# Performance work log

Measured on AMD Instinct MI355X. Metric: run time of the kernel, lower is better.

Reference implementation:

```python
import jax, jax.numpy as jnp
import numpy as np

B, S, D, H = 2, 2048, 1024, 16
HD = D // H


def setup_inputs() -> dict:
    key = jax.random.key(0)
    ks = jax.random.split(key, 5)
    scale = 0.02
    x = jax.random.normal(ks[0], (B, S, D), dtype=jnp.float32)
    Wq = jax.random.normal(ks[1], (D, D), dtype=jnp.float32) * scale
    Wk = jax.random.normal(ks[2], (D, D), dtype=jnp.float32) * scale
    Wv = jax.random.normal(ks[3], (D, D), dtype=jnp.float32) * scale
    Wo = jax.random.normal(ks[4], (D, D), dtype=jnp.float32) * scale
    z = jnp.zeros((D,), dtype=jnp.float32)
    return {"x": x, "Wq": Wq, "bq": z, "Wk": Wk, "bk": z, "Wv": Wv, "bv": z, "Wo": Wo, "bo": z}


def reference(x, Wq, bq, Wk, bk, Wv, bv, Wo, bo):
    b, s, d = x.shape
    hd = d // H
    # QKV projections -> [b, H, s, hd]
    def heads(W, bias):
        return (x @ W.T + bias).reshape(b, s, H, hd).transpose(0, 2, 1, 3)
    q = heads(Wq, bq)
    k = heads(Wk, bk)
    v = heads(Wv, bv)
    scale = 1.0 / np.sqrt(hd).astype(np.float32)
    attn = scale * jnp.einsum('bhqd,bhkd->bhqk', q, k)  # [b,H,s,s]
    # causal mask (attn dropout p=0 is identity before masking)
    causal = jnp.tril(jnp.ones((s, s), dtype=bool))
    attn = jnp.where(causal[None, None], attn, -jnp.inf)
    attn = jax.nn.softmax(attn, axis=-1)
    ans = jnp.einsum('bhqk,bhkd->bhqd', attn, v)
    ans = ans.transpose(0, 2, 1, 3).reshape(b, s, d)
    return ans @ Wo.T + bo
```

## Files before the change

### kernel.cpp

```cpp
#include <hip/hip_runtime.h>

#define DEV __device__ __forceinline__

typedef __attribute__((ext_vector_type(8))) __bf16 bf16x8;
typedef __attribute__((ext_vector_type(4))) float f32x4;
typedef __attribute__((ext_vector_type(16))) float f32x16;
typedef __attribute__((ext_vector_type(4))) unsigned short u16x4;
typedef __attribute__((ext_vector_type(8))) unsigned short u16x8;
typedef __attribute__((ext_vector_type(2))) unsigned u32x2;

DEV unsigned short f2bf(float f) {
  unsigned u = __builtin_bit_cast(unsigned, f);
  u += 0x7FFFu + ((u >> 16) & 1u);
  return (unsigned short)(u >> 16);
}

DEV f32x4 mfma16(bf16x8 a, bf16x8 b, f32x4 c) {
  return __builtin_amdgcn_mfma_f32_16x16x32_bf16(a, b, c, 0, 0, 0);
}
DEV f32x16 mfma32(bf16x8 a, bf16x8 b, f32x16 c) {
  return __builtin_amdgcn_mfma_f32_32x32x16_bf16(a, b, c, 0, 0, 0);
}

DEV void gload16(const void* g, void* l) {
  __builtin_amdgcn_global_load_lds(
      (const __attribute__((address_space(1))) unsigned int*)g,
      (__attribute__((address_space(3))) unsigned int*)l, 16, 0, 0);
}

DEV void plswap(unsigned& x, unsigned& y) {
#if __has_builtin(__builtin_amdgcn_permlane32_swap)
  u32x2 r = __builtin_amdgcn_permlane32_swap(x, y, false, false);
  x = r[0];
  y = r[1];
#else
  unsigned sx = __shfl_xor(x, 32, 64), sy = __shfl_xor(y, 32, 64);
  int hi = (threadIdx.x & 63) >> 5;
  unsigned nx = hi ? sy : x;
  unsigned ny = hi ? y : sx;
  x = nx;
  y = ny;
#endif
}
DEV float xadd32(float v) {
  unsigned a = __builtin_bit_cast(unsigned, v), b = a;
  plswap(a, b);
  return __builtin_bit_cast(float, a) + __builtin_bit_cast(float, b);
}

__global__ __launch_bounds__(256) void k_cvt_all(
    const float* __restrict__ x,
    const float* __restrict__ Wq, const float* __restrict__ Wk,
    const float* __restrict__ Wv, const float* __restrict__ Wo,
    unsigned short* __restrict__ xb,
    unsigned short* __restrict__ Wqb, unsigned short* __restrict__ Wkb,
    unsigned short* __restrict__ Wvb, unsigned short* __restrict__ Wob) {
  int g = blockIdx.x * 256 + threadIdx.x;
  const float* src;
  unsigned short* dst;
  int loc;
  if (g < 524288) {
    src = x; dst = xb; loc = g;
  } else {
    int r = g - 524288;
    int w = r >> 17;
    loc = r & 131071;
    src = w == 0 ? Wq : w == 1 ? Wk : w == 2 ? Wv : Wo;
    dst = w == 0 ? Wqb : w == 1 ? Wkb : w == 2 ? Wvb : Wob;
  }
  int row = loc >> 7, k8 = loc & 127;
  const f32x4* s = (const f32x4*)(src + ((size_t)row << 10) + (k8 << 3));
  f32x4 a = s[0], b = s[1];
  u16x8 o;
  o[0] = f2bf(a[0]); o[1] = f2bf(a[1]); o[2] = f2bf(a[2]); o[3] = f2bf(a[3]);
  o[4] = f2bf(b[0]); o[5] = f2bf(b[1]); o[6] = f2bf(b[2]); o[7] = f2bf(b[3]);
  *(u16x8*)(dst + ((size_t)row << 10) + ((k8 << 3) ^ ((row & 7) << 3))) = o;
}

DEV void gemm_mainloop(const char* Ag, const char* Bg, char* lds,
                       int lane, int wid, f32x4 acc[4][4]) {
  int g4 = lane >> 4, r16 = lane & 15;
  int wm = wid >> 1, wn = wid & 1;
  int adA[2], adB[2];
#pragma unroll
  for (int ks = 0; ks < 2; ++ks) {
    int swz = ((ks * 4 + g4) ^ (lane & 7)) << 4;
    adA[ks] = (wm * 64 + r16) * 128 + swz;
    adB[ks] = 16384 + (wn * 64 + r16) * 128 + swz;
  }
  int o0 = wid * 4096 + lane * 16;
  int grow[4], ginr[4];
#pragma unroll
  for (int i = 0; i < 4; ++i) {
    grow[i] = (o0 + i * 1024) >> 7;
    ginr[i] = (o0 + i * 1024) & 127;
  }
  auto STAGE = [&](int KT, int BASE) {
#pragma unroll
    for (int i = 0; i < 4; ++i) {
      int oo = o0 + i * 1024;
      size_t gofs = (size_t)grow[i] * 2048 + (size_t)KT * 128 + ginr[i];
      gload16(Ag + gofs, lds + BASE + oo);
      gload16(Bg + gofs, lds + BASE + 16384 + oo);
    }
  };
  STAGE(0, 0);
  __syncthreads();
  for (int kt = 0; kt < 16; ++kt) {
    int cur = (kt & 1) << 15;
    if (kt + 1 < 16) STAGE(kt + 1, cur ^ 32768);
#pragma unroll
    for (int ks = 0; ks < 2; ++ks) {
      bf16x8 af[4], bfr[4];
#pragma unroll
      for (int i = 0; i < 4; ++i) {
        af[i]  = *(const bf16x8*)(lds + cur + adA[ks] + i * 2048);
        bfr[i] = *(const bf16x8*)(lds + cur + adB[ks] + i * 2048);
      }
#pragma unroll
      for (int mi = 0; mi < 4; ++mi)
#pragma unroll
        for (int ni = 0; ni < 4; ++ni)
          acc[mi][ni] = mfma16(af[mi], bfr[ni], acc[mi][ni]);
    }
    __syncthreads();
  }
}

__global__ __launch_bounds__(256) void k_gemm_qkv(
    const unsigned short* __restrict__ xb,
    const unsigned short* __restrict__ Wqb, const unsigned short* __restrict__ Wkb,
    const unsigned short* __restrict__ Wvb,
    const float* __restrict__ bq, const float* __restrict__ bk,
    const float* __restrict__ bv,
    unsigned short* __restrict__ Qb, unsigned short* __restrict__ Kb,
    unsigned short* __restrict__ Vt) {
  __shared__ char lds[65536];
  int tid = threadIdx.x, lane = tid & 63, wid = tid >> 6;
  int bm = blockIdx.x & 31, bn = blockIdx.x >> 5;
  int r0 = bm * 128;
  int colT = bn * 128;
  int which = colT >> 10;
  int ncol = colT & 1023;
  const unsigned short* Wb = which == 0 ? Wqb : which == 1 ? Wkb : Wvb;
  f32x4 acc[4][4] = {};
  gemm_mainloop((const char*)xb + (size_t)r0 * 2048,
                (const char*)Wb + (size_t)ncol * 2048, lds, lane, wid, acc);
  int g4 = lane >> 4, r16 = lane & 15, wm = wid >> 1, wn = wid & 1;
  const float* bias = which == 0 ? bq : which == 1 ? bk : bv;
  float oscale = which == 0 ? 0.18033688f : 1.0f;
  int ncolw = ncol + wn * 64;
#pragma unroll
  for (int ni = 0; ni < 4; ++ni) {
    int gcol = ncolw + ni * 16 + r16;
    float bvv = bias[gcol];
    int h = gcol >> 6, hd = gcol & 63;
#pragma unroll
    for (int mi = 0; mi < 4; ++mi) {
      int growb = r0 + wm * 64 + mi * 16 + g4 * 4;
      int bb = growb >> 11, s0 = growb & 2047;
      if (which == 2) {
        u16x4 pk;
#pragma unroll
        for (int jj = 0; jj < 4; ++jj) pk[jj] = f2bf(acc[mi][ni][jj] + bvv);
        *(u16x4*)(Vt + ((size_t)(bb * 16 + h) * 64 + hd) * 2048 + s0) = pk;
      } else {
        unsigned short* dst = which == 0 ? Qb : Kb;
        size_t base = ((size_t)(bb * 16 + h) * 2048 + s0) * 64 + hd;
#pragma unroll
        for (int jj = 0; jj < 4; ++jj)
          dst[base + (size_t)jj * 64] = f2bf((acc[mi][ni][jj] + bvv) * oscale);
      }
    }
  }
}

__global__ __launch_bounds__(128) void k_attn(
    const unsigned short* __restrict__ Q, const unsigned short* __restrict__ K,
    const unsigned short* __restrict__ Vt, unsigned short* __restrict__ ansb,
    float* __restrict__ PO, float* __restrict__ PL) {
  __shared__ char lds[2 * 16384 + 256];
  int tid = threadIdx.x, lane = tid & 63, wid = tid >> 6;
  int l31 = lane & 31, hi = lane >> 5;
  int bid = blockIdx.x;
  int bh = (bid & 7) * 4 + ((bid >> 3) & 3);
  int s = bid >> 5;
  int c, t0, t1;
  bool direct;
  if (s < 16)      { c = 16 + s; t0 = 0;            t1 = (c + 2) >> 1; direct = false; }
  else if (s < 32) { c = s;      t0 = (c + 2) >> 1; t1 = c + 1;        direct = false; }
  else             { c = 47 - s; t0 = 0;            t1 = c + 1;        direct = true;  }
  int seg = (s < 32 && s >= 16) ? 1 : 0;
  int pidx = (bh * 16 + (c - 16)) * 2 + seg;
  int b = bh >> 4, h = bh & 15;
  int q0 = c * 64 + wid * 32;
  const unsigned short* Qh = Q + (size_t)bh * (2048 * 64);
  const char* Kg = (const char*)(K + (size_t)bh * (2048 * 64));
  const char* Vg = (const char*)(Vt + (size_t)bh * (64 * 2048));
  char* wb = lds + 32768 + wid * 128;

  int kof[4], ko[4], vo[4];
#pragma unroll
  for (int i = 0; i < 4; ++i) {
    int o = tid * 16 + i * 2048;
    int row = o >> 7, cc = o & 127;
    int sc = cc ^ ((row & 7) << 4);
    kof[i] = o;
    ko[i] = row * 128 + sc;
    vo[i] = row * 4096 + sc;
  }

  bf16x8 qf[4];
#pragma unroll
  for (int ks = 0; ks < 4; ++ks)
    qf[ks] = *(const bf16x8*)(Qh + (size_t)(q0 + l31) * 64 + ks * 16 + hi * 8);

  f32x16 O0 = {}, O1 = {}, l16 = {};
  int swzl = (l31 & 7) << 4;
  int hioff = hi * 16;

  auto STAGEA = [&](int T, int BASE) {
    size_t kK = (size_t)T * 8192;
    size_t kV = (size_t)T * 128;
#pragma unroll
    for (int i = 0; i < 4; ++i) {
      gload16(Kg + kK + ko[i], lds + BASE + kof[i]);
      gload16(Vg + kV + vo[i], lds + BASE + 8192 + kof[i]);
    }
  };

  STAGEA(t0, 0);
  __syncthreads();
  for (int t = t0; t < t1; ++t) {
    int cur = ((t - t0) & 1) << 14;
    if (t + 1 < t1) STAGEA(t + 1, cur ^ 16384);
    const char* KL = lds + cur;
    const char* VL = KL + 8192;
    f32x16 s0 = {}, s1 = {};
    __builtin_amdgcn_s_setprio(1);
#pragma unroll
    for (int ks = 0; ks < 4; ++ks) {
      bf16x8 kf0 = *(const bf16x8*)(KL + l31 * 128 + ((ks * 32 + hioff) ^ swzl));
      bf16x8 kf1 = *(const bf16x8*)(KL + (32 + l31) * 128 + ((ks * 32 + hioff) ^ swzl));
      s0 = mfma32(kf0, qf[ks], s0);
      s1 = mfma32(kf1, qf[ks], s1);
    }
    __builtin_amdgcn_s_setprio(0);
    if (t == c) {
      int lim2 = q0 + l31 - t * 64 - 4 * hi;
#pragma unroll
      for (int r = 0; r < 16; ++r) {
        int kc = (r & 3) + 8 * (r >> 2);
        if (kc > lim2) s0[r] = -1e30f;
        if (kc + 32 > lim2) s1[r] = -1e30f;
      }
    }
#pragma unroll
    for (int r = 0; r < 16; ++r) {
      s0[r] = __builtin_amdgcn_exp2f(s0[r]);
      s1[r] = __builtin_amdgcn_exp2f(s1[r]);
      l16[r] += s0[r] + s1[r];
    }
    __builtin_amdgcn_s_setprio(1);
#define PV_CHUNK(SV, E, C16) { \
    unsigned x0, x1, y0, y1; \
    asm("v_cvt_pk_bf16_f32 %0, %1, %2" : "=v"(x0) : "v"(SV[8*(E)+0]), "v"(SV[8*(E)+1])); \
    asm("v_cvt_pk_bf16_f32 %0, %1, %2" : "=v"(x1) : "v"(SV[8*(E)+2]), "v"(SV[8*(E)+3])); \
    asm("v_cvt_pk_bf16_f32 %0, %1, %2" : "=v"(y0) : "v"(SV[8*(E)+4]), "v"(SV[8*(E)+5])); \
    asm("v_cvt_pk_bf16_f32 %0, %1, %2" : "=v"(y1) : "v"(SV[8*(E)+6]), "v"(SV[8*(E)+7])); \
    plswap(x0, y0); \
    plswap(x1, y1); \
    union { unsigned u[4]; bf16x8 v; } pf; \
    pf.u[0] = x0; \
    pf.u[1] = x1; \
    pf.u[2] = y0; \
    pf.u[3] = y1; \
    bf16x8 v0 = *(const bf16x8*)(VL + l31 * 128 + (((C16) * 32 + hioff) ^ swzl)); \
    bf16x8 v1 = *(const bf16x8*)(VL + (32 + l31) * 128 + (((C16) * 32 + hioff) ^ swzl)); \
    O0 = mfma32(pf.v, v0, O0); \
    O1 = mfma32(pf.v, v1, O1); }
    PV_CHUNK(s0, 0, 0)
    PV_CHUNK(s0, 1, 1)
    PV_CHUNK(s1, 0, 2)
    PV_CHUNK(s1, 1, 3)
#undef PV_CHUNK
    __builtin_amdgcn_s_setprio(0);
    __syncthreads();
  }
  float a[16];
#pragma unroll
  for (int r = 0; r < 16; ++r) a[r] = l16[r];
#pragma unroll
  for (int st2 = 8; st2 >= 1; st2 >>= 1)
#pragma unroll
    for (int i = 0; i < st2; ++i) a[i] += a[i + st2];
  float lf = xadd32(a[0]);
  if (direct) {
    float rl = 1.f / lf;
    if (lane < 32) *(float*)(wb + l31 * 4) = rl;
    asm volatile("s_waitcnt lgkmcnt(0)" ::: "memory");
    f32x4 rv0 = *(const f32x4*)(wb + hioff);
    f32x4 rv1 = *(const f32x4*)(wb + 32 + hioff);
    f32x4 rv2 = *(const f32x4*)(wb + 64 + hioff);
    f32x4 rv3 = *(const f32x4*)(wb + 96 + hioff);
#pragma unroll
    for (int r = 0; r < 16; ++r) {
      float sc = (r < 4 ? rv0 : r < 8 ? rv1 : r < 12 ? rv2 : rv3)[r & 3];
      int rowl = q0 + (r & 3) + 8 * (r >> 2) + 4 * hi;
      int rowg = (b << 11) + rowl;
      int cswz = (rowl & 7) << 3;
      int cg0 = (h << 6) + l31;
      int cg1 = (h << 6) + 32 + l31;
      ansb[(size_t)rowg * 1024 + (cg0 ^ cswz)] = f2bf(O0[r] * sc);
      ansb[(size_t)rowg * 1024 + (cg1 ^ cswz)] = f2bf(O1[r] * sc);
    }
  } else {
    float* po = PO + (size_t)pidx * 4096;
#pragma unroll
    for (int r = 0; r < 16; ++r) {
      int rowl = wid * 32 + (r & 3) + 8 * (r >> 2) + 4 * hi;
      po[rowl * 64 + l31] = O0[r];
      po[rowl * 64 + 32 + l31] = O1[r];
    }
    if (hi == 0) PL[pidx * 64 + wid * 32 + l31] = lf;
  }
}

__global__ __launch_bounds__(256) void k_attn_combine(
    const float* __restrict__ PO, const float* __restrict__ PL,
    unsigned short* __restrict__ ansb) {
  int bid = blockIdx.x;
  int bh = bid & 31, cc = 16 + (bid >> 5);
  int b = bh >> 4, h = bh & 15;
  int t = threadIdx.x;
  int r = t >> 2, c4 = (t & 3) << 4;
  int pbase = (bh * 16 + (cc - 16)) * 2;
  const float* A = PO + (size_t)pbase * 4096 + r * 64 + c4;
  const float* B = A + 4096;
  float la = PL[pbase * 64 + r];
  float lb = PL[(pbase + 1) * 64 + r];
  float rl = 1.f / (la + lb);
  f32x4 s0 = *(const f32x4*)(A + 0) + *(const f32x4*)(B + 0);
  f32x4 s1 = *(const f32x4*)(A + 4) + *(const f32x4*)(B + 4);
  f32x4 s2 = *(const f32x4*)(A + 8) + *(const f32x4*)(B + 8);
  f32x4 s3 = *(const f32x4*)(A + 12) + *(const f32x4*)(B + 12);
  u16x8 o0, o1;
#pragma unroll
  for (int j = 0; j < 4; ++j) {
    o0[j] = f2bf(s0[j] * rl);
    o0[4 + j] = f2bf(s1[j] * rl);
    o1[j] = f2bf(s2[j] * rl);
    o1[4 + j] = f2bf(s3[j] * rl);
  }
  int rowg = (b << 11) + cc * 64 + r;
  int colg = (h << 6) + c4;
  int cswz = (rowg & 7) << 3;
  *(u16x8*)(ansb + (size_t)rowg * 1024 + (colg ^ cswz)) = o0;
  *(u16x8*)(ansb + (size_t)rowg * 1024 + ((colg + 8) ^ cswz)) = o1;
}

__global__ __launch_bounds__(256) void k_gemm_out(
    const unsigned short* __restrict__ ansb, const unsigned short* __restrict__ Wob,
    const float* __restrict__ bo, float* __restrict__ out) {
  __shared__ char lds[65536];
  int tid = threadIdx.x, lane = tid & 63, wid = tid >> 6;
  int bm = blockIdx.x & 31, bn = blockIdx.x >> 5;
  int r0 = bm * 128, c0 = bn * 128;
  f32x4 acc[4][4] = {};
  gemm_mainloop((const char*)ansb + (size_t)r0 * 2048,
                (const char*)Wob + (size_t)c0 * 2048, lds, lane, wid, acc);
  int g4 = lane >> 4, r16 = lane & 15, wm = wid >> 1, wn = wid & 1;
#pragma unroll
  for (int ni = 0; ni < 4; ++ni) {
    int gcol = c0 + wn * 64 + ni * 16 + r16;
    float bvv = bo[gcol];
#pragma unroll
    for (int mi = 0; mi < 4; ++mi) {
      int growb = r0 + wm * 64 + mi * 16 + g4 * 4;
#pragma unroll
      for (int jj = 0; jj < 4; ++jj)
        out[(size_t)(growb + jj) * 1024 + gcol] = acc[mi][ni][jj] + bvv;
    }
  }
}

extern "C" void kernel_launch(void* const* d_in, const int* in_sizes, int n_in,
                              void* d_out, int out_size, void* d_ws, size_t ws_size,
                              hipStream_t stream) {
  const float* x  = (const float*)d_in[0];
  const float* Wq = (const float*)d_in[1];
  const float* bq = (const float*)d_in[2];
  const float* Wk = (const float*)d_in[3];
  const float* bk = (const float*)d_in[4];
  const float* Wv = (const float*)d_in[5];
  const float* bv = (const float*)d_in[6];
  const float* Wo = (const float*)d_in[7];
  const float* bo = (const float*)d_in[8];
  char* ws = (char*)d_ws;
  unsigned short* xb   = (unsigned short*)(ws);
  unsigned short* ansb = (unsigned short*)(ws);
  unsigned short* Wqb  = (unsigned short*)(ws + (8u  << 20));
  unsigned short* Wkb  = (unsigned short*)(ws + (10u << 20));
  unsigned short* Wvb  = (unsigned short*)(ws + (12u << 20));
  unsigned short* Wob  = (unsigned short*)(ws + (14u << 20));
  unsigned short* Qb   = (unsigned short*)(ws + (16u << 20));
  unsigned short* Kb   = (unsigned short*)(ws + (24u << 20));
  unsigned short* Vt   = (unsigned short*)(ws + (32u << 20));
  float*          PO   = (float*)(ws + (40u << 20));
  float*          PL   = (float*)(ws + (56u << 20));

  k_cvt_all<<<4096, 256, 0, stream>>>(x, Wq, Wk, Wv, Wo, xb, Wqb, Wkb, Wvb, Wob);
  k_gemm_qkv<<<768, 256, 0, stream>>>(xb, Wqb, Wkb, Wvb, bq, bk, bv, Qb, Kb, Vt);
  k_attn<<<1536, 128, 0, stream>>>(Qb, Kb, Vt, ansb, PO, PL);
  k_attn_combine<<<512, 256, 0, stream>>>(PO, PL, ansb);
  k_gemm_out<<<256, 256, 0, stream>>>(ansb, Wob, bo, (float*)d_out);
}
```

Before: 107.5 us.

## Split causal attention rows into up to four KV segments; read V from global

Query tiles are now split across 1–4 key/value segments according to their causal length, which raises the attention grid from 1536 to 2560 blocks and balances per-block work more finely. The combine kernel sums a variable number of partial outputs and normalizers. V fragments are now loaded straight from global memory instead of being staged in LDS, which halves the LDS footprint per block and may raise occupancy. The trade-offs are more partial-result traffic, a heavier combine step, and uncached, less coalesced V reads on every iteration.

```diff
diff --git a/kernel.cpp b/kernel.cpp
--- a/kernel.cpp
+++ b/kernel.cpp
@@ -179,35 +179,34 @@
     const unsigned short* __restrict__ Q, const unsigned short* __restrict__ K,
     const unsigned short* __restrict__ Vt, unsigned short* __restrict__ ansb,
     float* __restrict__ PO, float* __restrict__ PL) {
-  __shared__ char lds[2 * 16384 + 256];
+  __shared__ char lds[2 * 8192 + 256];
   int tid = threadIdx.x, lane = tid & 63, wid = tid >> 6;
   int l31 = lane & 31, hi = lane >> 5;
   int bid = blockIdx.x;
   int bh = (bid & 7) * 4 + ((bid >> 3) & 3);
-  int s = bid >> 5;
-  int c, t0, t1;
-  bool direct;
-  if (s < 16)      { c = 16 + s; t0 = 0;            t1 = (c + 2) >> 1; direct = false; }
-  else if (s < 32) { c = s;      t0 = (c + 2) >> 1; t1 = c + 1;        direct = false; }
-  else             { c = 47 - s; t0 = 0;            t1 = c + 1;        direct = true;  }
-  int seg = (s < 32 && s >= 16) ? 1 : 0;
-  int pidx = (bh * 16 + (c - 16)) * 2 + seg;
+  int sden = bid >> 5;
+  int c, j, nseg;
+  if (sden < 8)       { c = sden; j = 0; nseg = 1; }
+  else if (sden < 24) { int u = sden - 8;  c = 8  + (u >> 1); j = u & 1; nseg = 2; }
+  else if (sden < 48) { int u = sden - 24; int q3 = u / 3; c = 16 + q3; j = u - 3 * q3; nseg = 3; }
+  else                { int u = sden - 48; c = 24 + (u >> 2); j = u & 3; nseg = 4; }
+  int t0 = j * (c + 1) / nseg, t1 = (j + 1) * (c + 1) / nseg;
+  bool direct = (nseg == 1);
+  int pidx = (bh * 24 + (c - 8)) * 4 + j;
   int b = bh >> 4, h = bh & 15;
   int q0 = c * 64 + wid * 32;
   const unsigned short* Qh = Q + (size_t)bh * (2048 * 64);
   const char* Kg = (const char*)(K + (size_t)bh * (2048 * 64));
   const char* Vg = (const char*)(Vt + (size_t)bh * (64 * 2048));
-  char* wb = lds + 32768 + wid * 128;
-
-  int kof[4], ko[4], vo[4];
+  char* wb = lds + 16384 + wid * 128;
+
+  int kof[4], ko[4];
 #pragma unroll
   for (int i = 0; i < 4; ++i) {
     int o = tid * 16 + i * 2048;
     int row = o >> 7, cc = o & 127;
-    int sc = cc ^ ((row & 7) << 4);
     kof[i] = o;
-    ko[i] = row * 128 + sc;
-    vo[i] = row * 4096 + sc;
+    ko[i] = row * 128 + (cc ^ ((row & 7) << 4));
   }
 
   bf16x8 qf[4];
@@ -218,24 +217,24 @@
   f32x16 O0 = {}, O1 = {}, l16 = {};
   int swzl = (l31 & 7) << 4;
   int hioff = hi * 16;
-
-  auto STAGEA = [&](int T, int BASE) {
+  const char* Vr0 = Vg + (size_t)l31 * 4096;
+  const char* Vr1 = Vg + (size_t)(32 + l31) * 4096;
+
+  auto STAGEK = [&](int T, int BASE) {
     size_t kK = (size_t)T * 8192;
-    size_t kV = (size_t)T * 128;
-#pragma unroll
-    for (int i = 0; i < 4; ++i) {
+#pragma unroll
+    for (int i = 0; i < 4; ++i)
       gload16(Kg + kK + ko[i], lds + BASE + kof[i]);
-      gload16(Vg + kV + vo[i], lds + BASE + 8192 + kof[i]);
-    }
   };
 
-  STAGEA(t0, 0);
+  STAGEK(t0, 0);
   __syncthreads();
   for (int t = t0; t < t1; ++t) {
-    int cur = ((t - t0) & 1) << 14;
-    if (t + 1 < t1) STAGEA(t + 1, cur ^ 16384);
+    int cur = ((t - t0) & 1) << 13;
+    if (t + 1 < t1) STAGEK(t + 1, cur ^ 8192);
     const char* KL = lds + cur;
-    const char* VL = KL + 8192;
+    const char* Vt0 = Vr0 + (size_t)t * 128;
+    const char* Vt1 = Vr1 + (size_t)t * 128;
     f32x16 s0 = {}, s1 = {};
     __builtin_amdgcn_s_setprio(1);
 #pragma unroll
@@ -275,8 +274,8 @@
     pf.u[1] = x1; \
     pf.u[2] = y0; \
     pf.u[3] = y1; \
-    bf16x8 v0 = *(const bf16x8*)(VL + l31 * 128 + (((C16) * 32 + hioff) ^ swzl)); \
-    bf16x8 v1 = *(const bf16x8*)(VL + (32 + l31) * 128 + (((C16) * 32 + hioff) ^ swzl)); \
+    bf16x8 v0 = *(const bf16x8*)(Vt0 + (C16) * 32 + hi * 16); \
+    bf16x8 v1 = *(const bf16x8*)(Vt1 + (C16) * 32 + hi * 16); \
     O0 = mfma32(pf.v, v0, O0); \
     O1 = mfma32(pf.v, v1, O1); }
     PV_CHUNK(s0, 0, 0)
@@ -330,20 +329,23 @@
     const float* __restrict__ PO, const float* __restrict__ PL,
     unsigned short* __restrict__ ansb) {
   int bid = blockIdx.x;
-  int bh = bid & 31, cc = 16 + (bid >> 5);
+  int bh = bid & 31, cc = 8 + (bid >> 5);
+  int nseg = cc < 16 ? 2 : cc < 24 ? 3 : 4;
   int b = bh >> 4, h = bh & 15;
   int t = threadIdx.x;
   int r = t >> 2, c4 = (t & 3) << 4;
-  int pbase = (bh * 16 + (cc - 16)) * 2;
-  const float* A = PO + (size_t)pbase * 4096 + r * 64 + c4;
-  const float* B = A + 4096;
-  float la = PL[pbase * 64 + r];
-  float lb = PL[(pbase + 1) * 64 + r];
-  float rl = 1.f / (la + lb);
-  f32x4 s0 = *(const f32x4*)(A + 0) + *(const f32x4*)(B + 0);
-  f32x4 s1 = *(const f32x4*)(A + 4) + *(const f32x4*)(B + 4);
-  f32x4 s2 = *(const f32x4*)(A + 8) + *(const f32x4*)(B + 8);
-  f32x4 s3 = *(const f32x4*)(A + 12) + *(const f32x4*)(B + 12);
+  int pbase = (bh * 24 + (cc - 8)) * 4;
+  f32x4 s0 = {}, s1 = {}, s2 = {}, s3 = {};
+  float lsum = 0.f;
+  for (int j = 0; j < nseg; ++j) {
+    const float* A = PO + (size_t)(pbase + j) * 4096 + r * 64 + c4;
+    s0 += *(const f32x4*)(A + 0);
+    s1 += *(const f32x4*)(A + 4);
+    s2 += *(const f32x4*)(A + 8);
+    s3 += *(const f32x4*)(A + 12);
+    lsum += PL[(pbase + j) * 64 + r];
+  }
+  float rl = 1.f / lsum;
   u16x8 o0, o1;
 #pragma unroll
   for (int j = 0; j < 4; ++j) {
@@ -407,11 +409,11 @@
   unsigned short* Kb   = (unsigned short*)(ws + (24u << 20));
   unsigned short* Vt   = (unsigned short*)(ws + (32u << 20));
   float*          PO   = (float*)(ws + (40u << 20));
-  float*          PL   = (float*)(ws + (56u << 20));
+  float*          PL   = (float*)(ws + (88u << 20));
 
   k_cvt_all<<<4096, 256, 0, stream>>>(x, Wq, Wk, Wv, Wo, xb, Wqb, Wkb, Wvb, Wob);
   k_gemm_qkv<<<768, 256, 0, stream>>>(xb, Wqb, Wkb, Wvb, bq, bk, bv, Qb, Kb, Vt);
-  k_attn<<<1536, 128, 0, stream>>>(Qb, Kb, Vt, ansb, PO, PL);
-  k_attn_combine<<<512, 256, 0, stream>>>(PO, PL, ansb);
+  k_attn<<<2560, 128, 0, stream>>>(Qb, Kb, Vt, ansb, PO, PL);
+  k_attn_combine<<<768, 256, 0, stream>>>(PO, PL, ansb);
   k_gemm_out<<<256, 256, 0, stream>>>(ansb, Wob, bo, (float*)d_out);
 }
```

Result: slower. 125.2 us (+16.4%).

## Stage K/V tiles in pairs and rebalance causal attention work segments

Applied to the files above, without the earlier changes.

The attention kernel now loads two 64-key K/V tiles per pipeline stage into a doubled LDS buffer and computes both before each barrier, halving the number of block-wide syncs. It also replaces the fixed two-way split of causal rows with a lookup table that assigns block segments of more even length. The larger LDS footprint (about 64KB per block) may reduce how many blocks fit per CU.

```diff
diff --git a/kernel.cpp b/kernel.cpp
--- a/kernel.cpp
+++ b/kernel.cpp
@@ -179,25 +179,35 @@
     const unsigned short* __restrict__ Q, const unsigned short* __restrict__ K,
     const unsigned short* __restrict__ Vt, unsigned short* __restrict__ ansb,
     float* __restrict__ PO, float* __restrict__ PL) {
-  __shared__ char lds[2 * 16384 + 256];
+  __shared__ char lds[2 * 32768 + 256];
+#define SG(c, a, bb2) ((unsigned)(c) | ((unsigned)(a) << 8) | ((unsigned)(bb2) << 16))
+  static const unsigned SEGT[48] = {
+    SG(30,0,16), SG(31,0,16), SG(31,16,32), SG(15,0,16),
+    SG(28,0,15), SG(29,0,15), SG(29,15,30), SG(30,16,31), SG(14,0,15),
+    SG(26,0,14), SG(27,0,14), SG(27,14,28), SG(28,15,29), SG(13,0,14),
+    SG(24,0,13), SG(25,0,13), SG(25,13,26), SG(26,14,27), SG(12,0,13),
+    SG(22,0,12), SG(23,0,12), SG(23,12,24), SG(24,13,25), SG(11,0,12),
+    SG(20,0,11), SG(21,0,11), SG(21,11,22), SG(22,12,23), SG(10,0,11),
+    SG(18,0,10), SG(19,0,10), SG(19,10,20), SG(20,11,21), SG(9,0,10),
+    SG(16,0,9),  SG(17,0,9),  SG(17,9,18),  SG(18,10,19), SG(8,0,9),
+    SG(16,9,17), SG(7,0,8), SG(6,0,7), SG(5,0,6), SG(4,0,5), SG(3,0,4),
+    SG(2,0,3), SG(1,0,2), SG(0,0,1)
+  };
+#undef SG
   int tid = threadIdx.x, lane = tid & 63, wid = tid >> 6;
   int l31 = lane & 31, hi = lane >> 5;
   int bid = blockIdx.x;
   int bh = (bid & 7) * 4 + ((bid >> 3) & 3);
-  int s = bid >> 5;
-  int c, t0, t1;
-  bool direct;
-  if (s < 16)      { c = 16 + s; t0 = 0;            t1 = (c + 2) >> 1; direct = false; }
-  else if (s < 32) { c = s;      t0 = (c + 2) >> 1; t1 = c + 1;        direct = false; }
-  else             { c = 47 - s; t0 = 0;            t1 = c + 1;        direct = true;  }
-  int seg = (s < 32 && s >= 16) ? 1 : 0;
-  int pidx = (bh * 16 + (c - 16)) * 2 + seg;
+  unsigned se = SEGT[bid >> 5];
+  int c = se & 255, t0 = (se >> 8) & 255, t1 = (se >> 16) & 255;
+  bool direct = (c < 16);
+  int pidx = (bh * 16 + (c - 16)) * 2 + (t0 != 0 ? 1 : 0);
   int b = bh >> 4, h = bh & 15;
   int q0 = c * 64 + wid * 32;
   const unsigned short* Qh = Q + (size_t)bh * (2048 * 64);
   const char* Kg = (const char*)(K + (size_t)bh * (2048 * 64));
   const char* Vg = (const char*)(Vt + (size_t)bh * (64 * 2048));
-  char* wb = lds + 32768 + wid * 128;
+  char* wb = lds + 65536 + wid * 128;
 
   int kof[4], ko[4], vo[4];
 #pragma unroll
@@ -219,23 +229,25 @@
   int swzl = (l31 & 7) << 4;
   int hioff = hi * 16;
 
-  auto STAGEA = [&](int T, int BASE) {
-    size_t kK = (size_t)T * 8192;
-    size_t kV = (size_t)T * 128;
+  auto STAGEP = [&](int P, int BASE) {
+    int t = t0 + 2 * P;
+    size_t kK = (size_t)t * 8192;
+    size_t kV = (size_t)t * 128;
 #pragma unroll
     for (int i = 0; i < 4; ++i) {
       gload16(Kg + kK + ko[i], lds + BASE + kof[i]);
       gload16(Vg + kV + vo[i], lds + BASE + 8192 + kof[i]);
     }
+    if (t + 1 < t1) {
+#pragma unroll
+      for (int i = 0; i < 4; ++i) {
+        gload16(Kg + kK + 8192 + ko[i], lds + BASE + 16384 + kof[i]);
+        gload16(Vg + kV + 128 + vo[i], lds + BASE + 24576 + kof[i]);
+      }
+    }
   };
 
-  STAGEA(t0, 0);
-  __syncthreads();
-  for (int t = t0; t < t1; ++t) {
-    int cur = ((t - t0) & 1) << 14;
-    if (t + 1 < t1) STAGEA(t + 1, cur ^ 16384);
-    const char* KL = lds + cur;
-    const char* VL = KL + 8192;
+  auto COMP = [&](int t, const char* KL, const char* VL) {
     f32x16 s0 = {}, s1 = {};
     __builtin_amdgcn_s_setprio(1);
 #pragma unroll
@@ -285,6 +297,17 @@
     PV_CHUNK(s1, 1, 3)
 #undef PV_CHUNK
     __builtin_amdgcn_s_setprio(0);
+  };
+
+  int npairs = (t1 - t0 + 1) >> 1;
+  STAGEP(0, 0);
+  __syncthreads();
+  for (int p = 0; p < npairs; ++p) {
+    int cur = (p & 1) << 15;
+    if (p + 1 < npairs) STAGEP(p + 1, cur ^ 32768);
+    int t = t0 + 2 * p;
+    COMP(t, lds + cur, lds + cur + 8192);
+    if (t + 1 < t1) COMP(t + 1, lds + cur + 16384, lds + cur + 24576);
     __syncthreads();
   }
   float a[16];
```

After: 113.9 us. +6.0%, slower.
